# Performance work log

Measured on AMD Instinct MI355X. Metric: run time of the kernel, lower is better.

## Reference

```python
import jax, jax.numpy as jnp
import numpy as np

B, T, D = 4, 1024, 1024
N, H = 16, 64  # num_heads, key_dim
SOFT_CAP = 50.0
R_SOFTPLUS_0 = 1.442695041


def setup_inputs() -> dict:
    key = jax.random.key(0)
    ks = jax.random.split(key, 12)
    s = 0.02
    return {
        "query": jax.random.normal(ks[0], (B, T, D), jnp.float32),
        "value": jax.random.normal(ks[1], (B, T, D), jnp.float32),
        "Wq": jax.random.normal(ks[2], (D, N, H), jnp.float32) * s,
        "bq": jnp.zeros((N, H), jnp.float32),
        "Wk": jax.random.normal(ks[3], (D, N, H), jnp.float32) * s,
        "bk": jnp.zeros((N, H), jnp.float32),
        "Wv": jax.random.normal(ks[4], (D, N, H), jnp.float32) * s,
        "bv": jnp.zeros((N, H), jnp.float32),
        "Wo": jax.random.normal(ks[5], (N, H, D), jnp.float32) * s,
        "bo": jnp.zeros((D,), jnp.float32),
        "per_dim_scale": jnp.zeros((H,), jnp.float32),
    }


def reference(query, value, Wq, bq, Wk, bk, Wv, bv, Wo, bo, per_dim_scale):
    # key defaults to query (self-attention)
    q = jnp.einsum("btd,dnh->btnh", query, Wq) + bq
    k = jnp.einsum("btd,dnh->btnh", query, Wk) + bk
    v = jnp.einsum("btd,dnh->btnh", value, Wv) + bv
    # per-dim scale: r_softplus_0 / sqrt(H) * softplus(per_dim_scale)
    scale = (R_SOFTPLUS_0 / jnp.sqrt(jnp.float32(H))) * jax.nn.softplus(per_dim_scale)
    q = q * scale
    score = jnp.einsum("btnh,bsnh->bnts", q, k)  # [B,N,T,T]
    score = SOFT_CAP * jnp.tanh(score / SOFT_CAP)
    weights = jax.nn.softmax(score.astype(jnp.float32), axis=-1)
    weights = weights.astype(q.dtype)
    context = jnp.einsum("bnts,bsnh->btnh", weights, v)
    out = jnp.einsum("btnh,nhd->btd", context, Wo) + bo
    return out
```

## Files before the change

### kernel.cpp

```cpp
#include <hip/hip_runtime.h>
#include <math.h>

#define M_TOT 4096
#define D_DIM 1024
#define NH    1024
#define N3    3072
#define T_DIM 1024

typedef __attribute__((ext_vector_type(8))) short bf16x8;
typedef __attribute__((ext_vector_type(4))) float f32x4;
typedef unsigned short u16;
typedef unsigned int   u32;

__device__ __forceinline__ u16 f2bf(float f) {
    u32 u = __float_as_uint(f);
    u32 r = (u + 0x7fffu + ((u >> 16) & 1u)) >> 16;
    return (u16)r;
}

__device__ __forceinline__ void gload16(const void* g, void* l) {
    __builtin_amdgcn_global_load_lds(
        (__attribute__((address_space(1))) void*)g,
        (__attribute__((address_space(3))) void*)l, 16, 0, 0);
}

__global__ __launch_bounds__(256) void cast_all_kernel(
    const float* __restrict__ query, const float* __restrict__ value,
    const float* __restrict__ Wq, const float* __restrict__ Wk,
    const float* __restrict__ Wv, const float* __restrict__ Wo,
    u16* __restrict__ xb, u16* __restrict__ wbT, u16* __restrict__ woT)
{
    const int blk = blockIdx.x;
    const int tid = threadIdx.x;
    if (blk < 8192) {
        const int z = blk >> 12;
        const float* __restrict__ src = z ? value : query;
        u16* dst = xb + (size_t)z * M_TOT * D_DIM;
        const size_t i4 = (size_t)(blk & 4095) * 256 + tid;
        float4 v = *reinterpret_cast<const float4*>(src + i4 * 4);
        ushort4 o;
        o.x = f2bf(v.x); o.y = f2bf(v.y); o.z = f2bf(v.z); o.w = f2bf(v.w);
        *reinterpret_cast<ushort4*>(dst + i4 * 4) = o;
        return;
    }
    const int idx = blk - 8192;
    const int z = idx >> 8;
    const int bx = idx & 15, by = (idx >> 4) & 15;
    const float* __restrict__ src = (z == 0) ? Wq : (z == 1) ? Wk : (z == 2) ? Wv : Wo;
    u16* dst = (z < 3) ? (wbT + (size_t)z * 1024 * 1024) : woT;
    __shared__ float ts[64][65];
    const int tx = tid & 15, ty = tid >> 4;
    const int c0 = bx * 64, d0 = by * 64;
    #pragma unroll
    for (int i = 0; i < 4; ++i) {
        int r = ty + i * 16;
        float4 v = *reinterpret_cast<const float4*>(&src[(size_t)(d0 + r) * 1024 + c0 + tx * 4]);
        ts[r][tx * 4 + 0] = v.x; ts[r][tx * 4 + 1] = v.y;
        ts[r][tx * 4 + 2] = v.z; ts[r][tx * 4 + 3] = v.w;
    }
    __syncthreads();
    #pragma unroll
    for (int i = 0; i < 4; ++i) {
        int r = ty + i * 16;
        ushort4 o;
        o.x = f2bf(ts[tx * 4 + 0][r]);
        o.y = f2bf(ts[tx * 4 + 1][r]);
        o.z = f2bf(ts[tx * 4 + 2][r]);
        o.w = f2bf(ts[tx * 4 + 3][r]);
        *reinterpret_cast<ushort4*>(&dst[(size_t)(c0 + r) * 1024 + d0 + tx * 4]) = o;
    }
}

__global__ __launch_bounds__(512) void gemm_qkv_kernel(
    const u16* __restrict__ xb, const u16* __restrict__ wbT,
    const float* __restrict__ bq, const float* __restrict__ bk,
    const float* __restrict__ bv, const float* __restrict__ pds,
    u16* __restrict__ qkv, u16* __restrict__ vt)
{
    __shared__ __align__(16) u16 Asl[3][128 * 32];
    __shared__ __align__(16) u16 Bsl[3][128 * 32];
    const int tid = threadIdx.x;
    const int l = tid & 63, w = tid >> 6, g = l >> 4;
    const int wr = w >> 2, wc = w & 3;
    const int disp = blockIdx.x + blockIdx.y * 24;
    const int logical = (disp & 7) * 96 + (disp >> 3);
    const int n0 = (logical % 24) * 128, m0 = (logical / 24) * 128;
    const u16* __restrict__ A = xb + ((n0 >= 2048) ? (size_t)M_TOT * D_DIM : 0);

    const int srow = w * 16 + (l >> 2);
    const int skel = (((l & 3) ^ ((srow >> 1) & 3)) * 8);

    f32x4 acc[4][2];
    #pragma unroll
    for (int i = 0; i < 4; ++i)
        #pragma unroll
        for (int j = 0; j < 2; ++j)
            acc[i][j] = (f32x4){0.f, 0.f, 0.f, 0.f};

    auto stage = [&](int buf, int k0) {
        gload16(&A  [(size_t)(m0 + srow) * 1024 + k0 + skel], &Asl[buf][w * 512]);
        gload16(&wbT[(size_t)(n0 + srow) * 1024 + k0 + skel], &Bsl[buf][w * 512]);
    };

    stage(0, 0);
    stage(1, 32);

    int cur = 0;
    for (int t = 0; t < 32; ++t) {
        if (t < 31) asm volatile("s_waitcnt vmcnt(2)" ::: "memory");
        else        asm volatile("s_waitcnt vmcnt(0)" ::: "memory");
        __builtin_amdgcn_s_barrier();
        __builtin_amdgcn_sched_barrier(0);
        if (t < 30) {
            int nbuf = cur + 2; if (nbuf >= 3) nbuf -= 3;
            stage(nbuf, (t + 2) * 32);
        }
        bf16x8 af[4], bfr[2];
        #pragma unroll
        for (int mf = 0; mf < 4; ++mf) {
            int row = wr * 64 + mf * 16 + (l & 15);
            af[mf] = *(const bf16x8*)((const char*)&Asl[cur][0] + row * 64 +
                      ((g ^ ((row >> 1) & 3)) << 4));
        }
        #pragma unroll
        for (int nf = 0; nf < 2; ++nf) {
            int row = wc * 32 + nf * 16 + (l & 15);
            bfr[nf] = *(const bf16x8*)((const char*)&Bsl[cur][0] + row * 64 +
                      ((g ^ ((row >> 1) & 3)) << 4));
        }
        #pragma unroll
        for (int mf = 0; mf < 4; ++mf)
            #pragma unroll
            for (int nf = 0; nf < 2; ++nf)
                acc[mf][nf] = __builtin_amdgcn_mfma_f32_16x16x32_bf16(
                    af[mf], bfr[nf], acc[mf][nf], 0, 0, 0);
        ++cur; if (cur == 3) cur = 0;
    }

    const int colb = n0 + wc * 32;
    const int rowb = m0 + wr * 64 + (l >> 4) * 4;
    #pragma unroll
    for (int nf = 0; nf < 2; ++nf) {
        const int col = colb + nf * 16 + (l & 15);
        float bias, scale = 1.0f;
        if (col < 1024) {
            bias = bq[col];
            float x = pds[col & 63];
            float sp = (x > 20.f) ? x : log1pf(expf(x));
            scale = 0.1803368801f * sp;
        } else if (col < 2048) {
            bias = bk[col - 1024];
        } else {
            bias = bv[col - 2048];
        }
        #pragma unroll
        for (int mf = 0; mf < 4; ++mf) {
            if (col < 2048) {
                #pragma unroll
                for (int r = 0; r < 4; ++r) {
                    int row = rowb + mf * 16 + r;
                    qkv[(size_t)row * N3 + col] = f2bf((acc[mf][nf][r] + bias) * scale);
                }
            } else {
                int b   = rowb >> 10;
                int s0r = (rowb + mf * 16) & 1023;
                int h = col & 63, nhd = (col >> 6) & 15;
                ushort4 o;
                o.x = f2bf(acc[mf][nf][0] + bias);
                o.y = f2bf(acc[mf][nf][1] + bias);
                o.z = f2bf(acc[mf][nf][2] + bias);
                o.w = f2bf(acc[mf][nf][3] + bias);
                *reinterpret_cast<ushort4*>(
                    &vt[(size_t)((b * 16 + nhd) * 64 + h) * 1024 + s0r]) = o;
            }
        }
    }
}

__global__ __launch_bounds__(512) void attn_mfma_kernel(
    const u16* __restrict__ qkv, const u16* __restrict__ vt,
    u16* __restrict__ ctx)
{
    __shared__ __align__(16) u16 Ks [2][64 * 64];
    __shared__ __align__(16) u16 Vts[2][64 * 64];
    __shared__ __align__(16) u16 Ps [128 * 64];
    const int tid = threadIdx.x;
    const int l = tid & 63, w = tid >> 6, g = l >> 4;
    const int disp = blockIdx.x + blockIdx.y * 8;
    const int logical = (disp & 7) * 64 + (disp >> 3);
    const int qt = logical & 7, bn = logical >> 3;
    const int b = bn >> 4, n = bn & 15;
    const int q0 = qt * 128;

    auto stage = [&](int buf, int s0) {
        int srow = w * 8 + (l >> 3);
        int qb   = (l & 7) * 16;
        int lb   = qb ^ ((srow & 7) << 4);
        gload16(&qkv[(size_t)(b * 1024 + s0 + srow) * N3 + 1024 + n * 64 + (lb >> 1)],
                &Ks[buf][w * 512]);
        gload16(&vt[(size_t)(bn * 64 + srow) * 1024 + s0 + (lb >> 1)],
                &Vts[buf][w * 512]);
    };

    stage(0, 0);

    bf16x8 qf[2];
    #pragma unroll
    for (int kh = 0; kh < 2; ++kh) {
        int row = b * 1024 + q0 + w * 16 + (l & 15);
        int col = n * 64 + kh * 32 + g * 8;
        qf[kh] = *(const bf16x8*)&qkv[(size_t)row * N3 + col];
    }

    bf16x8 ones;
    #pragma unroll
    for (int j = 0; j < 8; ++j) ones[j] = (short)0x3F80;

    f32x4 acc[4];
    f32x4 acc_d = (f32x4){0.f, 0.f, 0.f, 0.f};
    #pragma unroll
    for (int nf = 0; nf < 4; ++nf) acc[nf] = (f32x4){0.f, 0.f, 0.f, 0.f};

    char* const psb = (char*)Ps + w * 2048;

    const float C1 = 1.44269504f;
    const float C2 = -1.9235934e-4f;

    __syncthreads();

    for (int t = 0; t < 16; ++t) {
        const int cur = t & 1;
        if (t < 15) stage(cur ^ 1, (t + 1) * 64);

        f32x4 st[4];
        __builtin_amdgcn_s_setprio(1);
        #pragma unroll
        for (int sf = 0; sf < 4; ++sf) {
            int rowk = sf * 16 + (l & 15);
            const char* kbp = (const char*)Ks[cur] + rowk * 128;
            int sw = (rowk & 7) << 4;
            bf16x8 kb0 = *(const bf16x8*)(kbp + ((g * 16 +  0) ^ sw));
            bf16x8 kb1 = *(const bf16x8*)(kbp + ((g * 16 + 64) ^ sw));
            f32x4 z = (f32x4){0.f, 0.f, 0.f, 0.f};
            z = __builtin_amdgcn_mfma_f32_16x16x32_bf16(kb0, qf[0], z, 0, 0, 0);
            z = __builtin_amdgcn_mfma_f32_16x16x32_bf16(kb1, qf[1], z, 0, 0, 0);
            st[sf] = z;
        }
        __builtin_amdgcn_s_setprio(0);

        #pragma unroll
        for (int sf = 0; sf < 4; ++sf) {
            float p[4];
            #pragma unroll
            for (int r = 0; r < 4; ++r) {
                float sc = st[sf][r];
                float e = sc * fmaf(sc * sc, C2, C1);
                asm("v_exp_f32 %0, %1" : "=v"(p[r]) : "v"(e));
            }
            int row = l & 15;
            uint2 pk;
            asm("v_cvt_pk_bf16_f32 %0, %1, %2" : "=v"(pk.x) : "v"(p[0]), "v"(p[1]));
            asm("v_cvt_pk_bf16_f32 %0, %1, %2" : "=v"(pk.y) : "v"(p[2]), "v"(p[3]));
            *(uint2*)(psb + row * 128 + ((sf * 32 + g * 8) ^ ((row & 7) << 4))) = pk;
        }
        asm volatile("s_waitcnt lgkmcnt(0)");
        __builtin_amdgcn_sched_barrier(0);

        __builtin_amdgcn_s_setprio(1);
        #pragma unroll
        for (int ks = 0; ks < 2; ++ks) {
            int row = l & 15;
            bf16x8 pa = *(const bf16x8*)(psb + row * 128 +
                        ((ks * 64 + g * 16) ^ ((row & 7) << 4)));
            acc_d = __builtin_amdgcn_mfma_f32_16x16x32_bf16(pa, ones, acc_d, 0, 0, 0);
            #pragma unroll
            for (int nf = 0; nf < 4; ++nf) {
                int rowv = nf * 16 + (l & 15);
                bf16x8 vb = *(const bf16x8*)((const char*)Vts[cur] + rowv * 128 +
                          ((ks * 64 + g * 16) ^ ((rowv & 7) << 4)));
                acc[nf] = __builtin_amdgcn_mfma_f32_16x16x32_bf16(
                    pa, vb, acc[nf], 0, 0, 0);
            }
        }
        __builtin_amdgcn_s_setprio(0);
        __syncthreads();
    }

    float inv[4];
    #pragma unroll
    for (int r = 0; r < 4; ++r) inv[r] = 1.0f / acc_d[r];

    #pragma unroll
    for (int nf = 0; nf < 4; ++nf) {
        int col = n * 64 + nf * 16 + (l & 15);
        #pragma unroll
        for (int r = 0; r < 4; ++r) {
            int rl = w * 16 + g * 4 + r;
            ctx[(size_t)(b * 1024 + q0 + rl) * NH + col] = f2bf(acc[nf][r] * inv[r]);
        }
    }
}

__global__ __launch_bounds__(512) void gemm_out_kernel(
    const u16* __restrict__ ctx, const u16* __restrict__ woT,
    const float* __restrict__ bo, float* __restrict__ out)
{
    __shared__ __align__(16) u16 Asl[3][64 * 32];
    __shared__ __align__(16) u16 Bsl[3][128 * 32];
    const int tid = threadIdx.x;
    const int l = tid & 63, w = tid >> 6, g = l >> 4;
    const int wr = w >> 2, wc = w & 3;
    const int disp = blockIdx.x + blockIdx.y * 8;
    const int logical = (disp & 7) * 64 + (disp >> 3);
    const int n0 = (logical & 7) * 128, m0 = (logical >> 3) * 64;

    const int srow = w * 16 + (l >> 2);
    const int skel = (((l & 3) ^ ((srow >> 1) & 3)) * 8);

    f32x4 acc[2][2];
    #pragma unroll
    for (int i = 0; i < 2; ++i)
        #pragma unroll
        for (int j = 0; j < 2; ++j)
            acc[i][j] = (f32x4){0.f, 0.f, 0.f, 0.f};

    auto stage = [&](int buf, int k0) {
        gload16(&woT[(size_t)(n0 + srow) * 1024 + k0 + skel], &Bsl[buf][w * 512]);
        if (w < 4)
            gload16(&ctx[(size_t)(m0 + srow) * 1024 + k0 + skel], &Asl[buf][w * 512]);
    };

    stage(0, 0);
    stage(1, 32);

    int cur = 0;
    for (int t = 0; t < 32; ++t) {
        if (t < 31) asm volatile("s_waitcnt vmcnt(1)" ::: "memory");
        else        asm volatile("s_waitcnt vmcnt(0)" ::: "memory");
        __builtin_amdgcn_s_barrier();
        __builtin_amdgcn_sched_barrier(0);
        if (t < 30) {
            int nbuf = cur + 2; if (nbuf >= 3) nbuf -= 3;
            stage(nbuf, (t + 2) * 32);
        }
        bf16x8 af[2], bfr[2];
        #pragma unroll
        for (int mf = 0; mf < 2; ++mf) {
            int row = wr * 32 + mf * 16 + (l & 15);
            af[mf] = *(const bf16x8*)((const char*)&Asl[cur][0] + row * 64 +
                      ((g ^ ((row >> 1) & 3)) << 4));
        }
        #pragma unroll
        for (int nf = 0; nf < 2; ++nf) {
            int row = wc * 32 + nf * 16 + (l & 15);
            bfr[nf] = *(const bf16x8*)((const char*)&Bsl[cur][0] + row * 64 +
                      ((g ^ ((row >> 1) & 3)) << 4));
        }
        #pragma unroll
        for (int mf = 0; mf < 2; ++mf)
            #pragma unroll
            for (int nf = 0; nf < 2; ++nf)
                acc[mf][nf] = __builtin_amdgcn_mfma_f32_16x16x32_bf16(
                    af[mf], bfr[nf], acc[mf][nf], 0, 0, 0);
        ++cur; if (cur == 3) cur = 0;
    }

    const int colb = n0 + wc * 32;
    const int rowb = m0 + wr * 32 + (l >> 4) * 4;
    #pragma unroll
    for (int nf = 0; nf < 2; ++nf) {
        const int col = colb + nf * 16 + (l & 15);
        const float bias = bo[col];
        #pragma unroll
        for (int mf = 0; mf < 2; ++mf)
            #pragma unroll
            for (int r = 0; r < 4; ++r)
                out[(size_t)(rowb + mf * 16 + r) * 1024 + col] = acc[mf][nf][r] + bias;
    }
}

extern "C" void kernel_launch(void* const* d_in, const int* in_sizes, int n_in,
                              void* d_out, int out_size, void* d_ws, size_t ws_size,
                              hipStream_t stream) {
    const float* query = (const float*)d_in[0];
    const float* value = (const float*)d_in[1];
    const float* Wq    = (const float*)d_in[2];
    const float* bq    = (const float*)d_in[3];
    const float* Wk    = (const float*)d_in[4];
    const float* bk    = (const float*)d_in[5];
    const float* Wv    = (const float*)d_in[6];
    const float* bv    = (const float*)d_in[7];
    const float* Wo    = (const float*)d_in[8];
    const float* bo    = (const float*)d_in[9];
    const float* pds   = (const float*)d_in[10];
    float* out = (float*)d_out;

    char* ws = (char*)d_ws;
    u16* xb   = (u16*)(ws);
    u16* wbT  = (u16*)(ws + (16ull << 20));
    u16* woT  = (u16*)(ws + (22ull << 20));
    u16* qkv  = (u16*)(ws + (24ull << 20));
    u16* vt   = (u16*)(ws + (48ull << 20));
    u16* ctxb = (u16*)(ws + (56ull << 20));

    cast_all_kernel<<<dim3(9216), 256, 0, stream>>>(
        query, value, Wq, Wk, Wv, Wo, xb, wbT, woT);
    gemm_qkv_kernel<<<dim3(N3 / 128, M_TOT / 128), 512, 0, stream>>>(
        xb, wbT, bq, bk, bv, pds, qkv, vt);
    attn_mfma_kernel<<<dim3(T_DIM / 128, 64), 512, 0, stream>>>(qkv, vt, ctxb);
    gemm_out_kernel<<<dim3(NH / 128, M_TOT / 64), 512, 0, stream>>>(ctxb, woT, bo, out);
}
```

Baseline: 95.25 us.

## Fuse fp32-to-bf16 activation cast into QKV GEMM A-tile loading

Removes the separate pass that converts query/value to bf16 in workspace. The QKV GEMM now reads fp32 activations into registers, converts them with packed bf16 conversion instructions, and writes them to LDS, restructuring the pipeline to use register prefetch for A and 4 LDS buffers for B. This saves a full write and re-read of 16 MB of bf16 activations. In exchange each GEMM tile is converted redundantly across the 8 column blocks, twice the fp32 bytes are read from global memory, and each step pays extra barrier and waitcnt synchronisation.

Result: slower. 102.4 us (+7.5%).

```diff
diff --git a/kernel.cpp b/kernel.cpp
--- a/kernel.cpp
+++ b/kernel.cpp
@@ -24,33 +24,18 @@
         (__attribute__((address_space(3))) void*)l, 16, 0, 0);
 }
 
-__global__ __launch_bounds__(256) void cast_all_kernel(
-    const float* __restrict__ query, const float* __restrict__ value,
+__global__ __launch_bounds__(256) void cast_wt_kernel(
     const float* __restrict__ Wq, const float* __restrict__ Wk,
     const float* __restrict__ Wv, const float* __restrict__ Wo,
-    u16* __restrict__ xb, u16* __restrict__ wbT, u16* __restrict__ woT)
+    u16* __restrict__ wbT, u16* __restrict__ woT)
 {
-    const int blk = blockIdx.x;
-    const int tid = threadIdx.x;
-    if (blk < 8192) {
-        const int z = blk >> 12;
-        const float* __restrict__ src = z ? value : query;
-        u16* dst = xb + (size_t)z * M_TOT * D_DIM;
-        const size_t i4 = (size_t)(blk & 4095) * 256 + tid;
-        float4 v = *reinterpret_cast<const float4*>(src + i4 * 4);
-        ushort4 o;
-        o.x = f2bf(v.x); o.y = f2bf(v.y); o.z = f2bf(v.z); o.w = f2bf(v.w);
-        *reinterpret_cast<ushort4*>(dst + i4 * 4) = o;
-        return;
-    }
-    const int idx = blk - 8192;
-    const int z = idx >> 8;
-    const int bx = idx & 15, by = (idx >> 4) & 15;
+    const int z = blockIdx.z;
     const float* __restrict__ src = (z == 0) ? Wq : (z == 1) ? Wk : (z == 2) ? Wv : Wo;
     u16* dst = (z < 3) ? (wbT + (size_t)z * 1024 * 1024) : woT;
     __shared__ float ts[64][65];
+    const int tid = threadIdx.x;
     const int tx = tid & 15, ty = tid >> 4;
-    const int c0 = bx * 64, d0 = by * 64;
+    const int c0 = blockIdx.x * 64, d0 = blockIdx.y * 64;
     #pragma unroll
     for (int i = 0; i < 4; ++i) {
         int r = ty + i * 16;
@@ -72,23 +57,25 @@
 }
 
 __global__ __launch_bounds__(512) void gemm_qkv_kernel(
-    const u16* __restrict__ xb, const u16* __restrict__ wbT,
+    const float* __restrict__ query, const float* __restrict__ value,
+    const u16* __restrict__ wbT,
     const float* __restrict__ bq, const float* __restrict__ bk,
     const float* __restrict__ bv, const float* __restrict__ pds,
     u16* __restrict__ qkv, u16* __restrict__ vt)
 {
-    __shared__ __align__(16) u16 Asl[3][128 * 32];
-    __shared__ __align__(16) u16 Bsl[3][128 * 32];
+    __shared__ __align__(16) u16 Asl[2][128 * 32];
+    __shared__ __align__(16) u16 Bsl[4][128 * 32];
     const int tid = threadIdx.x;
     const int l = tid & 63, w = tid >> 6, g = l >> 4;
     const int wr = w >> 2, wc = w & 3;
     const int disp = blockIdx.x + blockIdx.y * 24;
     const int logical = (disp & 7) * 96 + (disp >> 3);
     const int n0 = (logical % 24) * 128, m0 = (logical / 24) * 128;
-    const u16* __restrict__ A = xb + ((n0 >= 2048) ? (size_t)M_TOT * D_DIM : 0);
-
-    const int srow = w * 16 + (l >> 2);
-    const int skel = (((l & 3) ^ ((srow >> 1) & 3)) * 8);
+    const float* __restrict__ Af = (n0 >= 2048) ? value : query;
+
+    const int arow  = w * 16 + (l >> 2);
+    const int aphys = (l & 3) ^ ((arow >> 1) & 3);
+    const int skelB = (((l & 3) ^ ((arow >> 1) & 3)) * 8);
 
     f32x4 acc[4][2];
     #pragma unroll
@@ -97,45 +84,78 @@
         for (int j = 0; j < 2; ++j)
             acc[i][j] = (f32x4){0.f, 0.f, 0.f, 0.f};
 
-    auto stage = [&](int buf, int k0) {
-        gload16(&A  [(size_t)(m0 + srow) * 1024 + k0 + skel], &Asl[buf][w * 512]);
-        gload16(&wbT[(size_t)(n0 + srow) * 1024 + k0 + skel], &Bsl[buf][w * 512]);
-    };
-
-    stage(0, 0);
-    stage(1, 32);
-
-    int cur = 0;
-    for (int t = 0; t < 32; ++t) {
-        if (t < 31) asm volatile("s_waitcnt vmcnt(2)" ::: "memory");
-        else        asm volatile("s_waitcnt vmcnt(0)" ::: "memory");
-        __builtin_amdgcn_s_barrier();
-        __builtin_amdgcn_sched_barrier(0);
-        if (t < 30) {
-            int nbuf = cur + 2; if (nbuf >= 3) nbuf -= 3;
-            stage(nbuf, (t + 2) * 32);
-        }
-        bf16x8 af[4], bfr[2];
-        #pragma unroll
-        for (int mf = 0; mf < 4; ++mf) {
-            int row = wr * 64 + mf * 16 + (l & 15);
-            af[mf] = *(const bf16x8*)((const char*)&Asl[cur][0] + row * 64 +
-                      ((g ^ ((row >> 1) & 3)) << 4));
-        }
-        #pragma unroll
-        for (int nf = 0; nf < 2; ++nf) {
-            int row = wc * 32 + nf * 16 + (l & 15);
-            bfr[nf] = *(const bf16x8*)((const char*)&Bsl[cur][0] + row * 64 +
-                      ((g ^ ((row >> 1) & 3)) << 4));
-        }
-        #pragma unroll
-        for (int mf = 0; mf < 4; ++mf)
-            #pragma unroll
-            for (int nf = 0; nf < 2; ++nf)
-                acc[mf][nf] = __builtin_amdgcn_mfma_f32_16x16x32_bf16(
-                    af[mf], bfr[nf], acc[mf][nf], 0, 0, 0);
-        ++cur; if (cur == 3) cur = 0;
-    }
+    float4 aw0lo, aw0hi, aw1lo, aw1hi;
+
+    gload16(&wbT[(size_t)(n0 + arow) * 1024 + 0 + skelB], &Bsl[0][w * 512]);
+    {
+        const float* ap = &Af[(size_t)(m0 + arow) * 1024 + 0 + (l & 3) * 8];
+        aw0lo = *(const float4*)ap; aw0hi = *(const float4*)(ap + 4);
+    }
+    gload16(&wbT[(size_t)(n0 + arow) * 1024 + 32 + skelB], &Bsl[1][w * 512]);
+    {
+        const float* ap = &Af[(size_t)(m0 + arow) * 1024 + 32 + (l & 3) * 8];
+        aw1lo = *(const float4*)ap; aw1hi = *(const float4*)(ap + 4);
+    }
+    asm volatile("s_waitcnt vmcnt(3)" ::: "memory");
+    {
+        u32 q0_, q1_, q2_, q3_;
+        asm("v_cvt_pk_bf16_f32 %0, %1, %2" : "=v"(q0_) : "v"(aw0lo.x), "v"(aw0lo.y));
+        asm("v_cvt_pk_bf16_f32 %0, %1, %2" : "=v"(q1_) : "v"(aw0lo.z), "v"(aw0lo.w));
+        asm("v_cvt_pk_bf16_f32 %0, %1, %2" : "=v"(q2_) : "v"(aw0hi.x), "v"(aw0hi.y));
+        asm("v_cvt_pk_bf16_f32 %0, %1, %2" : "=v"(q3_) : "v"(aw0hi.z), "v"(aw0hi.w));
+        uint4 pk; pk.x = q0_; pk.y = q1_; pk.z = q2_; pk.w = q3_;
+        *(uint4*)((char*)&Asl[0][0] + arow * 64 + aphys * 16) = pk;
+    }
+    asm volatile("s_waitcnt lgkmcnt(0)" ::: "memory");
+    __builtin_amdgcn_sched_barrier(0);
+    __builtin_amdgcn_s_barrier();
+
+#define QKV_STEP(T, BBc, ABc, ISSLO, ISSHI, CONSLO, CONSHI) do {               \
+    if ((T) + 2 < 32) {                                                        \
+        gload16(&wbT[(size_t)(n0 + arow) * 1024 + ((T) + 2) * 32 + skelB],     \
+                &Bsl[((BBc) + 2) & 3][w * 512]);                               \
+        const float* ap_ = &Af[(size_t)(m0 + arow) * 1024 + ((T) + 2) * 32 + (l & 3) * 8]; \
+        ISSLO = *(const float4*)ap_; ISSHI = *(const float4*)(ap_ + 4);        \
+        asm volatile("s_waitcnt vmcnt(3)" ::: "memory");                       \
+    } else if ((T) + 2 == 32) {                                                \
+        asm volatile("s_waitcnt vmcnt(0)" ::: "memory");                       \
+    }                                                                          \
+    if ((T) < 31) {                                                            \
+        u32 q0_, q1_, q2_, q3_;                                                \
+        asm("v_cvt_pk_bf16_f32 %0, %1, %2" : "=v"(q0_) : "v"(CONSLO.x), "v"(CONSLO.y)); \
+        asm("v_cvt_pk_bf16_f32 %0, %1, %2" : "=v"(q1_) : "v"(CONSLO.z), "v"(CONSLO.w)); \
+        asm("v_cvt_pk_bf16_f32 %0, %1, %2" : "=v"(q2_) : "v"(CONSHI.x), "v"(CONSHI.y)); \
+        asm("v_cvt_pk_bf16_f32 %0, %1, %2" : "=v"(q3_) : "v"(CONSHI.z), "v"(CONSHI.w)); \
+        uint4 pk_; pk_.x = q0_; pk_.y = q1_; pk_.z = q2_; pk_.w = q3_;         \
+        *(uint4*)((char*)&Asl[(ABc) ^ 1][0] + arow * 64 + aphys * 16) = pk_;   \
+    }                                                                          \
+    bf16x8 af_[4], bf_[2];                                                     \
+    _Pragma("unroll") for (int mf = 0; mf < 4; ++mf) {                         \
+        int row_ = wr * 64 + mf * 16 + (l & 15);                               \
+        af_[mf] = *(const bf16x8*)((const char*)&Asl[ABc][0] + row_ * 64 +     \
+                   ((g ^ ((row_ >> 1) & 3)) << 4));                            \
+    }                                                                          \
+    _Pragma("unroll") for (int nf = 0; nf < 2; ++nf) {                         \
+        int row_ = wc * 32 + nf * 16 + (l & 15);                               \
+        bf_[nf] = *(const bf16x8*)((const char*)&Bsl[BBc][0] + row_ * 64 +     \
+                   ((g ^ ((row_ >> 1) & 3)) << 4));                            \
+    }                                                                          \
+    _Pragma("unroll") for (int mf = 0; mf < 4; ++mf)                           \
+        _Pragma("unroll") for (int nf = 0; nf < 2; ++nf)                       \
+            acc[mf][nf] = __builtin_amdgcn_mfma_f32_16x16x32_bf16(             \
+                af_[mf], bf_[nf], acc[mf][nf], 0, 0, 0);                       \
+    asm volatile("s_waitcnt lgkmcnt(0)" ::: "memory");                         \
+    __builtin_amdgcn_sched_barrier(0);                                         \
+    __builtin_amdgcn_s_barrier();                                              \
+} while (0)
+
+    for (int tb = 0; tb < 32; tb += 4) {
+        QKV_STEP(tb + 0, 0, 0, aw0lo, aw0hi, aw1lo, aw1hi);
+        QKV_STEP(tb + 1, 1, 1, aw1lo, aw1hi, aw0lo, aw0hi);
+        QKV_STEP(tb + 2, 2, 0, aw0lo, aw0hi, aw1lo, aw1hi);
+        QKV_STEP(tb + 3, 3, 1, aw1lo, aw1hi, aw0lo, aw0hi);
+    }
+#undef QKV_STEP
 
     const int colb = n0 + wc * 32;
     const int rowb = m0 + wr * 64 + (l >> 4) * 4;
@@ -396,17 +416,15 @@
     float* out = (float*)d_out;
 
     char* ws = (char*)d_ws;
-    u16* xb   = (u16*)(ws);
-    u16* wbT  = (u16*)(ws + (16ull << 20));
-    u16* woT  = (u16*)(ws + (22ull << 20));
-    u16* qkv  = (u16*)(ws + (24ull << 20));
-    u16* vt   = (u16*)(ws + (48ull << 20));
-    u16* ctxb = (u16*)(ws + (56ull << 20));
-
-    cast_all_kernel<<<dim3(9216), 256, 0, stream>>>(
-        query, value, Wq, Wk, Wv, Wo, xb, wbT, woT);
+    u16* wbT  = (u16*)(ws);
+    u16* woT  = (u16*)(ws + ( 6ull << 20));
+    u16* qkv  = (u16*)(ws + ( 8ull << 20));
+    u16* vt   = (u16*)(ws + (32ull << 20));
+    u16* ctxb = (u16*)(ws + (40ull << 20));
+
+    cast_wt_kernel<<<dim3(16, 16, 4), 256, 0, stream>>>(Wq, Wk, Wv, Wo, wbT, woT);
     gemm_qkv_kernel<<<dim3(N3 / 128, M_TOT / 128), 512, 0, stream>>>(
-        xb, wbT, bq, bk, bv, pds, qkv, vt);
+        query, value, wbT, bq, bk, bv, pds, qkv, vt);
     attn_mfma_kernel<<<dim3(T_DIM / 128, 64), 512, 0, stream>>>(qkv, vt, ctxb);
     gemm_out_kernel<<<dim3(NH / 128, M_TOT / 64), 512, 0, stream>>>(ctxb, woT, bo, out);
 }
```

## Double query rows per attention block and triple-buffer K/V staging

Applied to the files above, without the earlier changes.

Each attention workgroup now handles 256 query rows instead of 128, with every wave processing two 16-row query fragments that share each loaded K and V fragment. The K/Vt LDS staging moves from double to triple buffering, prefetching two tiles ahead and using one vmcnt wait plus a single barrier per iteration instead of a trailing syncthreads. This halves K/V traffic per query and the number of syncs, at the cost of half as many workgroups (256), more registers and more LDS.

Measured after the change: 99.02 us. +4.0%, slower.

```diff
diff --git a/kernel.cpp b/kernel.cpp
--- a/kernel.cpp
+++ b/kernel.cpp
@@ -181,16 +181,28 @@
     const u16* __restrict__ qkv, const u16* __restrict__ vt,
     u16* __restrict__ ctx)
 {
-    __shared__ __align__(16) u16 Ks [2][64 * 64];
-    __shared__ __align__(16) u16 Vts[2][64 * 64];
-    __shared__ __align__(16) u16 Ps [128 * 64];
+    __shared__ __align__(16) u16 Ks [3][64 * 64];
+    __shared__ __align__(16) u16 Vts[3][64 * 64];
+    __shared__ __align__(16) u16 Ps [256 * 64];
     const int tid = threadIdx.x;
     const int l = tid & 63, w = tid >> 6, g = l >> 4;
-    const int disp = blockIdx.x + blockIdx.y * 8;
-    const int logical = (disp & 7) * 64 + (disp >> 3);
-    const int qt = logical & 7, bn = logical >> 3;
+    const int disp = blockIdx.x + blockIdx.y * 4;
+    const int logical = (disp & 7) * 32 + (disp >> 3);
+    const int qt = logical & 3, bn = logical >> 2;
     const int b = bn >> 4, n = bn & 15;
-    const int q0 = qt * 128;
+    const int q0 = qt * 256;
+
+    bf16x8 qf[2][2];
+    #pragma unroll
+    for (int qi = 0; qi < 2; ++qi)
+        #pragma unroll
+        for (int kh = 0; kh < 2; ++kh) {
+            int row = b * 1024 + q0 + w * 32 + qi * 16 + (l & 15);
+            int col = n * 64 + kh * 32 + g * 8;
+            qf[qi][kh] = *(const bf16x8*)&qkv[(size_t)row * N3 + col];
+        }
+    asm volatile("s_waitcnt vmcnt(0)" ::: "memory");
+    __builtin_amdgcn_sched_barrier(0);
 
     auto stage = [&](int buf, int s0) {
         int srow = w * 8 + (l >> 3);
@@ -203,36 +215,38 @@
     };
 
     stage(0, 0);
-
-    bf16x8 qf[2];
-    #pragma unroll
-    for (int kh = 0; kh < 2; ++kh) {
-        int row = b * 1024 + q0 + w * 16 + (l & 15);
-        int col = n * 64 + kh * 32 + g * 8;
-        qf[kh] = *(const bf16x8*)&qkv[(size_t)row * N3 + col];
-    }
+    stage(1, 64);
 
     bf16x8 ones;
     #pragma unroll
     for (int j = 0; j < 8; ++j) ones[j] = (short)0x3F80;
 
-    f32x4 acc[4];
-    f32x4 acc_d = (f32x4){0.f, 0.f, 0.f, 0.f};
-    #pragma unroll
-    for (int nf = 0; nf < 4; ++nf) acc[nf] = (f32x4){0.f, 0.f, 0.f, 0.f};
-
-    char* const psb = (char*)Ps + w * 2048;
+    f32x4 acc[2][4];
+    f32x4 acc_d[2];
+    #pragma unroll
+    for (int qi = 0; qi < 2; ++qi) {
+        acc_d[qi] = (f32x4){0.f, 0.f, 0.f, 0.f};
+        #pragma unroll
+        for (int nf = 0; nf < 4; ++nf) acc[qi][nf] = (f32x4){0.f, 0.f, 0.f, 0.f};
+    }
+
+    char* const psb = (char*)Ps + w * 4096;
 
     const float C1 = 1.44269504f;
     const float C2 = -1.9235934e-4f;
 
-    __syncthreads();
-
+    int cur = 0;
     for (int t = 0; t < 16; ++t) {
-        const int cur = t & 1;
-        if (t < 15) stage(cur ^ 1, (t + 1) * 64);
-
-        f32x4 st[4];
+        if (t < 15) asm volatile("s_waitcnt vmcnt(2)" ::: "memory");
+        else        asm volatile("s_waitcnt vmcnt(0)" ::: "memory");
+        __builtin_amdgcn_s_barrier();
+        __builtin_amdgcn_sched_barrier(0);
+        if (t < 14) {
+            int nbuf = cur + 2; if (nbuf >= 3) nbuf -= 3;
+            stage(nbuf, (t + 2) * 64);
+        }
+
+        f32x4 st[4][2];
         __builtin_amdgcn_s_setprio(1);
         #pragma unroll
         for (int sf = 0; sf < 4; ++sf) {
@@ -241,62 +255,76 @@
             int sw = (rowk & 7) << 4;
             bf16x8 kb0 = *(const bf16x8*)(kbp + ((g * 16 +  0) ^ sw));
             bf16x8 kb1 = *(const bf16x8*)(kbp + ((g * 16 + 64) ^ sw));
-            f32x4 z = (f32x4){0.f, 0.f, 0.f, 0.f};
-            z = __builtin_amdgcn_mfma_f32_16x16x32_bf16(kb0, qf[0], z, 0, 0, 0);
-            z = __builtin_amdgcn_mfma_f32_16x16x32_bf16(kb1, qf[1], z, 0, 0, 0);
-            st[sf] = z;
+            #pragma unroll
+            for (int qi = 0; qi < 2; ++qi) {
+                f32x4 z = (f32x4){0.f, 0.f, 0.f, 0.f};
+                z = __builtin_amdgcn_mfma_f32_16x16x32_bf16(kb0, qf[qi][0], z, 0, 0, 0);
+                z = __builtin_amdgcn_mfma_f32_16x16x32_bf16(kb1, qf[qi][1], z, 0, 0, 0);
+                st[sf][qi] = z;
+            }
         }
         __builtin_amdgcn_s_setprio(0);
 
         #pragma unroll
-        for (int sf = 0; sf < 4; ++sf) {
-            float p[4];
-            #pragma unroll
-            for (int r = 0; r < 4; ++r) {
-                float sc = st[sf][r];
-                float e = sc * fmaf(sc * sc, C2, C1);
-                asm("v_exp_f32 %0, %1" : "=v"(p[r]) : "v"(e));
-            }
-            int row = l & 15;
-            uint2 pk;
-            asm("v_cvt_pk_bf16_f32 %0, %1, %2" : "=v"(pk.x) : "v"(p[0]), "v"(p[1]));
-            asm("v_cvt_pk_bf16_f32 %0, %1, %2" : "=v"(pk.y) : "v"(p[2]), "v"(p[3]));
-            *(uint2*)(psb + row * 128 + ((sf * 32 + g * 8) ^ ((row & 7) << 4))) = pk;
-        }
+        for (int qi = 0; qi < 2; ++qi)
+            #pragma unroll
+            for (int sf = 0; sf < 4; ++sf) {
+                float p[4];
+                #pragma unroll
+                for (int r = 0; r < 4; ++r) {
+                    float sc = st[sf][qi][r];
+                    float e = sc * fmaf(sc * sc, C2, C1);
+                    asm("v_exp_f32 %0, %1" : "=v"(p[r]) : "v"(e));
+                }
+                int row = qi * 16 + (l & 15);
+                uint2 pk;
+                asm("v_cvt_pk_bf16_f32 %0, %1, %2" : "=v"(pk.x) : "v"(p[0]), "v"(p[1]));
+                asm("v_cvt_pk_bf16_f32 %0, %1, %2" : "=v"(pk.y) : "v"(p[2]), "v"(p[3]));
+                *(uint2*)(psb + row * 128 + ((sf * 32 + g * 8) ^ ((row & 7) << 4))) = pk;
+            }
         asm volatile("s_waitcnt lgkmcnt(0)");
         __builtin_amdgcn_sched_barrier(0);
 
         __builtin_amdgcn_s_setprio(1);
         #pragma unroll
         for (int ks = 0; ks < 2; ++ks) {
-            int row = l & 15;
-            bf16x8 pa = *(const bf16x8*)(psb + row * 128 +
-                        ((ks * 64 + g * 16) ^ ((row & 7) << 4)));
-            acc_d = __builtin_amdgcn_mfma_f32_16x16x32_bf16(pa, ones, acc_d, 0, 0, 0);
+            bf16x8 pa[2];
+            #pragma unroll
+            for (int qi = 0; qi < 2; ++qi) {
+                int row = qi * 16 + (l & 15);
+                pa[qi] = *(const bf16x8*)(psb + row * 128 +
+                          ((ks * 64 + g * 16) ^ ((row & 7) << 4)));
+                acc_d[qi] = __builtin_amdgcn_mfma_f32_16x16x32_bf16(
+                    pa[qi], ones, acc_d[qi], 0, 0, 0);
+            }
             #pragma unroll
             for (int nf = 0; nf < 4; ++nf) {
                 int rowv = nf * 16 + (l & 15);
                 bf16x8 vb = *(const bf16x8*)((const char*)Vts[cur] + rowv * 128 +
                           ((ks * 64 + g * 16) ^ ((rowv & 7) << 4)));
-                acc[nf] = __builtin_amdgcn_mfma_f32_16x16x32_bf16(
-                    pa, vb, acc[nf], 0, 0, 0);
+                #pragma unroll
+                for (int qi = 0; qi < 2; ++qi)
+                    acc[qi][nf] = __builtin_amdgcn_mfma_f32_16x16x32_bf16(
+                        pa[qi], vb, acc[qi][nf], 0, 0, 0);
             }
         }
         __builtin_amdgcn_s_setprio(0);
-        __syncthreads();
-    }
-
-    float inv[4];
-    #pragma unroll
-    for (int r = 0; r < 4; ++r) inv[r] = 1.0f / acc_d[r];
-
-    #pragma unroll
-    for (int nf = 0; nf < 4; ++nf) {
-        int col = n * 64 + nf * 16 + (l & 15);
-        #pragma unroll
-        for (int r = 0; r < 4; ++r) {
-            int rl = w * 16 + g * 4 + r;
-            ctx[(size_t)(b * 1024 + q0 + rl) * NH + col] = f2bf(acc[nf][r] * inv[r]);
+        ++cur; if (cur == 3) cur = 0;
+    }
+
+    #pragma unroll
+    for (int qi = 0; qi < 2; ++qi) {
+        float inv[4];
+        #pragma unroll
+        for (int r = 0; r < 4; ++r) inv[r] = 1.0f / acc_d[qi][r];
+        #pragma unroll
+        for (int nf = 0; nf < 4; ++nf) {
+            int col = n * 64 + nf * 16 + (l & 15);
+            #pragma unroll
+            for (int r = 0; r < 4; ++r) {
+                int rl = w * 32 + qi * 16 + g * 4 + r;
+                ctx[(size_t)(b * 1024 + q0 + rl) * NH + col] = f2bf(acc[qi][nf][r] * inv[r]);
+            }
         }
     }
 }
@@ -407,6 +435,6 @@
         query, value, Wq, Wk, Wv, Wo, xb, wbT, woT);
     gemm_qkv_kernel<<<dim3(N3 / 128, M_TOT / 128), 512, 0, stream>>>(
         xb, wbT, bq, bk, bv, pds, qkv, vt);
-    attn_mfma_kernel<<<dim3(T_DIM / 128, 64), 512, 0, stream>>>(qkv, vt, ctxb);
+    attn_mfma_kernel<<<dim3(T_DIM / 256, 64), 512, 0, stream>>>(qkv, vt, ctxb);
     gemm_out_kernel<<<dim3(NH / 128, M_TOT / 64), 512, 0, stream>>>(ctxb, woT, bo, out);
 }
```

## Keep P in registers for PV MFMA and triple-buffer K/V staging

Applied to the files above, without the earlier changes.

The attention kernel now feeds the bf16 probabilities directly from registers into 16x16x16 MFMAs, using the S^T fragment layout as the A operand. This removes the LDS round trip for P and the extra ones-matrix MFMA for the row sum, which is replaced by a scalar accumulation plus a cross-lane shuffle and a small shared array. K/V staging moves from double to triple buffering with vmcnt-based waits and one barrier per iteration. The trade-off is more LDS for K/V and hand-placed waits and nops that must be correct for the hazards. The 16x16x16 MFMA also needs twice as many instructions for the PV product.

Result: slower. 97.29 us (+2.1%).

```diff
diff --git a/kernel.cpp b/kernel.cpp
--- a/kernel.cpp
+++ b/kernel.cpp
@@ -8,6 +8,7 @@
 #define T_DIM 1024
 
 typedef __attribute__((ext_vector_type(8))) short bf16x8;
+typedef __attribute__((ext_vector_type(4))) short bf16x4;
 typedef __attribute__((ext_vector_type(4))) float f32x4;
 typedef unsigned short u16;
 typedef unsigned int   u32;
@@ -22,6 +23,11 @@
     __builtin_amdgcn_global_load_lds(
         (__attribute__((address_space(1))) void*)g,
         (__attribute__((address_space(3))) void*)l, 16, 0, 0);
+}
+
+__device__ __forceinline__ f32x4 mfma16(bf16x4 a, bf16x4 b, f32x4 c) {
+    asm("v_mfma_f32_16x16x16_bf16 %0, %1, %2, %0" : "+v"(c) : "v"(a), "v"(b));
+    return c;
 }
 
 __global__ __launch_bounds__(256) void cast_all_kernel(
@@ -181,9 +187,9 @@
     const u16* __restrict__ qkv, const u16* __restrict__ vt,
     u16* __restrict__ ctx)
 {
-    __shared__ __align__(16) u16 Ks [2][64 * 64];
-    __shared__ __align__(16) u16 Vts[2][64 * 64];
-    __shared__ __align__(16) u16 Ps [128 * 64];
+    __shared__ __align__(16) u16 Ks [3][64 * 64];
+    __shared__ __align__(16) u16 Vts[3][64 * 64];
+    __shared__ float dsh[128];
     const int tid = threadIdx.x;
     const int l = tid & 63, w = tid >> 6, g = l >> 4;
     const int disp = blockIdx.x + blockIdx.y * 8;
@@ -191,6 +197,16 @@
     const int qt = logical & 7, bn = logical >> 3;
     const int b = bn >> 4, n = bn & 15;
     const int q0 = qt * 128;
+
+    bf16x8 qf[2];
+    #pragma unroll
+    for (int kh = 0; kh < 2; ++kh) {
+        int row = b * 1024 + q0 + w * 16 + (l & 15);
+        int col = n * 64 + kh * 32 + g * 8;
+        qf[kh] = *(const bf16x8*)&qkv[(size_t)row * N3 + col];
+    }
+    asm volatile("s_waitcnt vmcnt(0)" ::: "memory");
+    __builtin_amdgcn_sched_barrier(0);
 
     auto stage = [&](int buf, int s0) {
         int srow = w * 8 + (l >> 3);
@@ -203,34 +219,26 @@
     };
 
     stage(0, 0);
-
-    bf16x8 qf[2];
-    #pragma unroll
-    for (int kh = 0; kh < 2; ++kh) {
-        int row = b * 1024 + q0 + w * 16 + (l & 15);
-        int col = n * 64 + kh * 32 + g * 8;
-        qf[kh] = *(const bf16x8*)&qkv[(size_t)row * N3 + col];
-    }
-
-    bf16x8 ones;
-    #pragma unroll
-    for (int j = 0; j < 8; ++j) ones[j] = (short)0x3F80;
+    stage(1, 64);
 
     f32x4 acc[4];
-    f32x4 acc_d = (f32x4){0.f, 0.f, 0.f, 0.f};
     #pragma unroll
     for (int nf = 0; nf < 4; ++nf) acc[nf] = (f32x4){0.f, 0.f, 0.f, 0.f};
-
-    char* const psb = (char*)Ps + w * 2048;
+    float dsum = 0.f;
 
     const float C1 = 1.44269504f;
     const float C2 = -1.9235934e-4f;
 
-    __syncthreads();
-
+    int cur = 0;
     for (int t = 0; t < 16; ++t) {
-        const int cur = t & 1;
-        if (t < 15) stage(cur ^ 1, (t + 1) * 64);
+        if (t < 15) asm volatile("s_waitcnt vmcnt(2)" ::: "memory");
+        else        asm volatile("s_waitcnt vmcnt(0)" ::: "memory");
+        __builtin_amdgcn_s_barrier();
+        __builtin_amdgcn_sched_barrier(0);
+        if (t < 14) {
+            int nbuf = cur + 2; if (nbuf >= 3) nbuf -= 3;
+            stage(nbuf, (t + 2) * 64);
+        }
 
         f32x4 st[4];
         __builtin_amdgcn_s_setprio(1);
@@ -248,6 +256,7 @@
         }
         __builtin_amdgcn_s_setprio(0);
 
+        uint2 pk[4];
         #pragma unroll
         for (int sf = 0; sf < 4; ++sf) {
             float p[4];
@@ -257,38 +266,40 @@
                 float e = sc * fmaf(sc * sc, C2, C1);
                 asm("v_exp_f32 %0, %1" : "=v"(p[r]) : "v"(e));
             }
-            int row = l & 15;
-            uint2 pk;
-            asm("v_cvt_pk_bf16_f32 %0, %1, %2" : "=v"(pk.x) : "v"(p[0]), "v"(p[1]));
-            asm("v_cvt_pk_bf16_f32 %0, %1, %2" : "=v"(pk.y) : "v"(p[2]), "v"(p[3]));
-            *(uint2*)(psb + row * 128 + ((sf * 32 + g * 8) ^ ((row & 7) << 4))) = pk;
-        }
-        asm volatile("s_waitcnt lgkmcnt(0)");
+            dsum += (p[0] + p[1]) + (p[2] + p[3]);
+            asm("v_cvt_pk_bf16_f32 %0, %1, %2" : "=v"(pk[sf].x) : "v"(p[0]), "v"(p[1]));
+            asm("v_cvt_pk_bf16_f32 %0, %1, %2" : "=v"(pk[sf].y) : "v"(p[2]), "v"(p[3]));
+        }
         __builtin_amdgcn_sched_barrier(0);
+        asm volatile("s_nop 7");
 
         __builtin_amdgcn_s_setprio(1);
         #pragma unroll
-        for (int ks = 0; ks < 2; ++ks) {
-            int row = l & 15;
-            bf16x8 pa = *(const bf16x8*)(psb + row * 128 +
-                        ((ks * 64 + g * 16) ^ ((row & 7) << 4)));
-            acc_d = __builtin_amdgcn_mfma_f32_16x16x32_bf16(pa, ones, acc_d, 0, 0, 0);
+        for (int sf = 0; sf < 4; ++sf) {
+            bf16x4 pa = __builtin_bit_cast(bf16x4, pk[sf]);
             #pragma unroll
             for (int nf = 0; nf < 4; ++nf) {
                 int rowv = nf * 16 + (l & 15);
-                bf16x8 vb = *(const bf16x8*)((const char*)Vts[cur] + rowv * 128 +
-                          ((ks * 64 + g * 16) ^ ((rowv & 7) << 4)));
-                acc[nf] = __builtin_amdgcn_mfma_f32_16x16x32_bf16(
-                    pa, vb, acc[nf], 0, 0, 0);
+                uint2 vraw = *(const uint2*)((const char*)Vts[cur] + rowv * 128 +
+                             ((sf * 32 + g * 8) ^ ((rowv & 7) << 4)));
+                acc[nf] = mfma16(pa, __builtin_bit_cast(bf16x4, vraw), acc[nf]);
             }
         }
         __builtin_amdgcn_s_setprio(0);
-        __syncthreads();
-    }
-
-    float inv[4];
-    #pragma unroll
-    for (int r = 0; r < 4; ++r) inv[r] = 1.0f / acc_d[r];
+        ++cur; if (cur == 3) cur = 0;
+    }
+
+    __builtin_amdgcn_sched_barrier(0);
+    asm volatile("s_nop 7\n\ts_nop 7");
+
+    {
+        float d = dsum;
+        d += __shfl_xor(d, 16);
+        d += __shfl_xor(d, 32);
+        if (l < 16) dsh[w * 16 + l] = 1.0f / d;
+    }
+    asm volatile("s_waitcnt lgkmcnt(0)" ::: "memory");
+    __builtin_amdgcn_sched_barrier(0);
 
     #pragma unroll
     for (int nf = 0; nf < 4; ++nf) {
@@ -296,7 +307,8 @@
         #pragma unroll
         for (int r = 0; r < 4; ++r) {
             int rl = w * 16 + g * 4 + r;
-            ctx[(size_t)(b * 1024 + q0 + rl) * NH + col] = f2bf(acc[nf][r] * inv[r]);
+            float inv = dsh[rl];
+            ctx[(size_t)(b * 1024 + q0 + rl) * NH + col] = f2bf(acc[nf][r] * inv);
         }
     }
 }
```
